# Kernel optimization log

Hardware: AMD Instinct MI355X
Metric: run time of the kernel (lower is better)

The kernel has to match this reference:

```python
import jax, jax.numpy as jnp
import numpy as np

B, S, D, H = 4, 2048, 1024, 16
DK = D // H


def setup_inputs() -> dict:
    key = jax.random.key(0)
    ks = jax.random.split(key, 12)
    scale = 1.0 / np.sqrt(D)
    inp = {
        "query": jax.random.normal(ks[0], (B, S, D), jnp.float32),
        "key": jax.random.normal(ks[1], (B, S, D), jnp.float32),
        "value": jax.random.normal(ks[2], (B, S, D), jnp.float32),
        # lower-triangular causal mask broadcast over batch (1 = keep, 0 = masked)
        "mask": jnp.broadcast_to(jnp.tril(jnp.ones((S, S), jnp.bool_)), (B, S, S)),
        "wq": jax.random.normal(ks[3], (D, D), jnp.float32) * scale,
        "bq": jnp.zeros((D,), jnp.float32),
        "wk": jax.random.normal(ks[4], (D, D), jnp.float32) * scale,
        "bk": jnp.zeros((D,), jnp.float32),
        "wv": jax.random.normal(ks[5], (D, D), jnp.float32) * scale,
        "bv": jnp.zeros((D,), jnp.float32),
        "wo": jax.random.normal(ks[6], (D, D), jnp.float32) * scale,
        "bo": jnp.zeros((D,), jnp.float32),
    }
    return inp


def _split_heads(x):
    # [B, S, D] -> [B, H, S, DK]
    return x.reshape(B, S, H, DK).transpose(0, 2, 1, 3)


def reference(query, key, value, mask, wq, bq, wk, bk, wv, bv, wo, bo):
    # torch.nn.Linear: y = x @ W.T + b
    q = _split_heads(query @ wq.T + bq)
    k = _split_heads(key @ wk.T + bk)
    v = _split_heads(value @ wv.T + bv)

    scores = jnp.einsum("bhqd,bhkd->bhqk", q, k) / jnp.sqrt(jnp.float32(DK))
    # mask.unsqueeze(1): [B,1,S,S] broadcast over heads; masked_fill(mask==0, -1e9)
    scores = jnp.where(mask[:, None, :, :], scores, jnp.float32(-1e9))
    attn = jax.nn.softmax(scores, axis=-1)
    # dropout is identity in eval/reference mode

    ctx = jnp.einsum("bhqk,bhkd->bhqd", attn, v)  # [B,H,S,DK]
    ctx = ctx.transpose(0, 2, 1, 3).reshape(B, S, D)
    return ctx @ wo.T + bo
```

## Files before the change

kernel.cpp:

```cpp
#include <hip/hip_runtime.h>
#include <hip/hip_bf16.h>
#include <hip/hip_fp16.h>

#define B_  4
#define S_  2048
#define D_  1024
#define H_  16
#define DK_ 64

#define DT_F32  0
#define DT_BF16 1
#define DT_F16  2

typedef __bf16 bf16x8 __attribute__((ext_vector_type(8)));
typedef float  f32x4  __attribute__((ext_vector_type(4)));

__device__ __forceinline__ float bf2f(unsigned short u) {
    return __uint_as_float(((unsigned int)u) << 16);
}
__device__ __forceinline__ unsigned short f2bf(float f) {
    unsigned int u = __float_as_uint(f);
    return (unsigned short)((u + 0x7FFFu + ((u >> 16) & 1u)) >> 16);
}
__device__ __forceinline__ float h2f(unsigned short u) {
    union { __half h; unsigned short s; } cv; cv.s = u;
    return __half2float(cv.h);
}
__device__ __forceinline__ unsigned short f2h(float f) {
    union { __half h; unsigned short s; } cv; cv.h = __float2half(f);
    return cv.s;
}

__device__ __forceinline__ void gld_lds16(const void* g, void* l) {
    __builtin_amdgcn_global_load_lds(
        (const __attribute__((address_space(1))) void*)g,
        (__attribute__((address_space(3))) void*)l, 16, 0, 0);
}

template<int DT>
__device__ __forceinline__ float4 ld4(const void* base, size_t idx) {
    if constexpr (DT == DT_F32) {
        return *(const float4*)((const float*)base + idx);
    } else if constexpr (DT == DT_BF16) {
        ushort4 u = *(const ushort4*)((const unsigned short*)base + idx);
        return make_float4(bf2f(u.x), bf2f(u.y), bf2f(u.z), bf2f(u.w));
    } else {
        ushort4 u = *(const ushort4*)((const unsigned short*)base + idx);
        return make_float4(h2f(u.x), h2f(u.y), h2f(u.z), h2f(u.w));
    }
}
template<int DT>
__device__ __forceinline__ float ld1(const void* base, size_t idx) {
    if constexpr (DT == DT_F32)  return ((const float*)base)[idx];
    if constexpr (DT == DT_BF16) return bf2f(((const unsigned short*)base)[idx]);
    return h2f(((const unsigned short*)base)[idx]);
}

__global__ void detect_dtype(const unsigned short* __restrict__ q,
                             int* __restrict__ flag) {
    int c_bf = 0, c_hi = 0;
    for (int i = 0; i < 256; ++i) {
        const int e = (q[i] >> 7) & 0xFF;
        c_bf += (e >= 100 && e <= 140);
        c_hi += (e > 140);
    }
    *flag = (c_hi > 16) ? DT_F32 : ((c_bf >= 250) ? DT_BF16 : DT_F16);
}

__global__ __launch_bounds__(256) void convW(
    const float* __restrict__ wq, const float* __restrict__ wk,
    const float* __restrict__ wv,
    const float* __restrict__ bq, const float* __restrict__ bk,
    const float* __restrict__ bv,
    unsigned short* __restrict__ Wc, unsigned short* __restrict__ Bc,
    const int* __restrict__ flag)
{
    if (*flag != DT_F32) return;
    const size_t NW = (size_t)D_ * D_;
    const size_t i = (size_t)blockIdx.x * blockDim.x + threadIdx.x;
    if (i * 4 < NW) {
        const float* src[3] = {wq, wk, wv};
        #pragma unroll
        for (int j = 0; j < 3; ++j) {
            float4 f = ((const float4*)src[j])[i];
            ushort4 u; u.x = f2bf(f.x); u.y = f2bf(f.y); u.z = f2bf(f.z); u.w = f2bf(f.w);
            ((ushort4*)(Wc + j * NW))[i] = u;
        }
    }
    if (i * 4 < D_) {
        const float* src[3] = {bq, bk, bv};
        #pragma unroll
        for (int j = 0; j < 3; ++j) {
            float4 f = ((const float4*)src[j])[i];
            ushort4 u; u.x = f2bf(f.x); u.y = f2bf(f.y); u.z = f2bf(f.z); u.w = f2bf(f.w);
            ((ushort4*)(Bc + j * D_))[i] = u;
        }
    }
}

__global__ __launch_bounds__(256) void conv3(
    const float* __restrict__ a, unsigned short* __restrict__ da, size_t na,
    const float* __restrict__ w, unsigned short* __restrict__ dw, size_t nw,
    const float* __restrict__ b, unsigned short* __restrict__ db, size_t nb,
    const int* __restrict__ flag)
{
    if (*flag != DT_F32) return;
    const size_t i = (size_t)blockIdx.x * blockDim.x + threadIdx.x;
    if (i * 4 < na) {
        float4 f = ((const float4*)a)[i];
        ushort4 u; u.x = f2bf(f.x); u.y = f2bf(f.y); u.z = f2bf(f.z); u.w = f2bf(f.w);
        ((ushort4*)da)[i] = u;
    }
    if (i * 4 < nw) {
        float4 f = ((const float4*)w)[i];
        ushort4 u; u.x = f2bf(f.x); u.y = f2bf(f.y); u.z = f2bf(f.z); u.w = f2bf(f.w);
        ((ushort4*)dw)[i] = u;
    }
    if (i * 4 < nb) {
        float4 f = ((const float4*)b)[i];
        ushort4 u; u.x = f2bf(f.x); u.y = f2bf(f.y); u.z = f2bf(f.z); u.w = f2bf(f.w);
        ((ushort4*)db)[i] = u;
    }
}

template<bool AF32>
__device__ __forceinline__ void gemm_qkv_body(
    const void* __restrict__ X, const unsigned short* __restrict__ W,
    const unsigned short* __restrict__ Bi, unsigned short* __restrict__ Y,
    const int zmode, const int m0, const int n0)
{
    __shared__ __align__(16) unsigned short Ash[128 * 32];
    __shared__ __align__(16) unsigned short Bsh[256 * 32];
    const int tid  = threadIdx.x;
    const int wv   = tid >> 6, lane = tid & 63;
    const int quad = lane >> 4, l16 = lane & 15;
    const int wm   = wv >> 2,  wn   = wv & 3;
    const int srow = lane >> 2, sc4 = lane & 3;

    f32x4 acc[4][4];
    #pragma unroll
    for (int nt = 0; nt < 4; ++nt) {
        const float bb = bf2f(Bi[n0 + wn * 64 + nt * 16 + l16]);
        #pragma unroll
        for (int mt = 0; mt < 4; ++mt) acc[mt][nt] = (f32x4){bb, bb, bb, bb};
    }

    for (int kt = 0; kt < 32; ++kt) {
        #pragma unroll
        for (int ph = 0; ph < 2; ++ph) {
            const int i   = wv + ph * 8;
            const int row = i * 16 + srow;
            gld_lds16(W + (size_t)(n0 + row) * D_ + kt * 32 + sc4 * 8,
                      (char*)Bsh + i * 1024);
        }
        {
            const int row = wv * 16 + srow;
            unsigned short* dst = Ash + wv * 512 + lane * 8;
            if constexpr (AF32) {
                const float* src = (const float*)X + (size_t)(m0 + row) * D_ + kt * 32 + sc4 * 8;
                const float4 a0 = ((const float4*)src)[0];
                const float4 a1 = ((const float4*)src)[1];
                bf16x8 vv;
                vv[0] = (__bf16)a0.x; vv[1] = (__bf16)a0.y;
                vv[2] = (__bf16)a0.z; vv[3] = (__bf16)a0.w;
                vv[4] = (__bf16)a1.x; vv[5] = (__bf16)a1.y;
                vv[6] = (__bf16)a1.z; vv[7] = (__bf16)a1.w;
                *(bf16x8*)dst = vv;
            } else {
                *(bf16x8*)dst = *(const bf16x8*)(
                    (const unsigned short*)X + (size_t)(m0 + row) * D_ + kt * 32 + sc4 * 8);
            }
        }
        __syncthreads();

        bf16x8 af[4], bfr[4];
        #pragma unroll
        for (int t = 0; t < 4; ++t) {
            af[t]  = *(const bf16x8*)(Ash + (wm * 64 + t * 16 + l16) * 32 + quad * 8);
            bfr[t] = *(const bf16x8*)(Bsh + (wn * 64 + t * 16 + l16) * 32 + quad * 8);
        }
        #pragma unroll
        for (int mt = 0; mt < 4; ++mt)
            #pragma unroll
            for (int nt = 0; nt < 4; ++nt)
                acc[mt][nt] = __builtin_amdgcn_mfma_f32_16x16x32_bf16(
                    af[mt], bfr[nt], acc[mt][nt], 0, 0, 0);
        __syncthreads();
    }

    #pragma unroll
    for (int mt = 0; mt < 4; ++mt) {
        const int mb = m0 + wm * 64 + mt * 16 + quad * 4;
        #pragma unroll
        for (int nt = 0; nt < 4; ++nt) {
            const int n = n0 + wn * 64 + nt * 16 + l16;
            const f32x4 a = acc[mt][nt];
            const int h = n >> 6, dk = n & 63;
            if (zmode != 2) {
                #pragma unroll
                for (int r = 0; r < 4; ++r) {
                    const int m = mb + r, b = m >> 11, s = m & (S_ - 1);
                    Y[(((size_t)(b * H_ + h) * S_ + s) << 6) + dk] = f2bf(a[r]);
                }
            } else {
                const int b = mb >> 11, s = mb & (S_ - 1);
                ushort4 u;
                u.x = f2bf(a[0]); u.y = f2bf(a[1]); u.z = f2bf(a[2]); u.w = f2bf(a[3]);
                *(ushort4*)(Y + (((size_t)(b * H_ + h) * DK_ + dk) << 11) + s) = u;
            }
        }
    }
}

__global__ __launch_bounds__(512) void gemm_qkv(
    const float* __restrict__ xq, const float* __restrict__ xk,
    const float* __restrict__ xv,
    const unsigned short* __restrict__ Wc,
    const unsigned short* __restrict__ wqb, const unsigned short* __restrict__ wkb,
    const unsigned short* __restrict__ wvb,
    const unsigned short* __restrict__ Bc,
    const unsigned short* __restrict__ bqb, const unsigned short* __restrict__ bkb,
    const unsigned short* __restrict__ bvb,
    unsigned short* __restrict__ Ybase,
    const int* __restrict__ flag)
{
    const int f = *flag;
    if (f == DT_F16) return;
    const int zz = blockIdx.z;
    const int n0 = blockIdx.x * 256;
    const int m0 = blockIdx.y * 128;

    const size_t NE = (size_t)B_ * S_ * D_;
    const size_t NW = (size_t)D_ * D_;
    unsigned short* Y = Ybase + (size_t)zz * NE;
    if (f == DT_F32) {
        const void* X = (zz == 0) ? (const void*)xq : (zz == 1) ? (const void*)xk : (const void*)xv;
        gemm_qkv_body<true>(X, Wc + (size_t)zz * NW, Bc + (size_t)zz * D_, Y, zz, m0, n0);
    } else {
        const void* X = (zz == 0) ? (const void*)xq : (zz == 1) ? (const void*)xk : (const void*)xv;
        const unsigned short* W  = (zz == 0) ? wqb : (zz == 1) ? wkb : wvb;
        const unsigned short* Bi = (zz == 0) ? bqb : (zz == 1) ? bkb : bvb;
        gemm_qkv_body<false>(X, W, Bi, Y, zz, m0, n0);
    }
}

__global__ __launch_bounds__(256) void gemm_out(
    const unsigned short* __restrict__ X,
    const unsigned short* __restrict__ Wa, const unsigned short* __restrict__ Wb,
    const unsigned short* __restrict__ Ba, const unsigned short* __restrict__ Bb,
    void* __restrict__ Y,
    const int* __restrict__ flag)
{
    const int f = *flag;
    if (f == DT_F16) return;
    const unsigned short* W  = (f == DT_F32) ? Wa : Wb;
    const unsigned short* Bi = (f == DT_F32) ? Ba : Bb;

    __shared__ __align__(16) unsigned short Ash[128 * 32];
    __shared__ __align__(16) unsigned short Bsh[128 * 32];
    const int tid  = threadIdx.x;
    const int wv   = tid >> 6, lane = tid & 63;
    const int quad = lane >> 4, l16 = lane & 15;
    const int wm   = wv >> 1,  wn   = wv & 1;
    const int srow = lane >> 2, sc4 = lane & 3;
    const int n0 = blockIdx.x * 128;
    const int m0 = blockIdx.y * 128;

    f32x4 acc[4][4];
    #pragma unroll
    for (int nt = 0; nt < 4; ++nt) {
        const float bb = bf2f(Bi[n0 + wn * 64 + nt * 16 + l16]);
        #pragma unroll
        for (int mt = 0; mt < 4; ++mt) acc[mt][nt] = (f32x4){bb, bb, bb, bb};
    }

    for (int kt = 0; kt < 32; ++kt) {
        #pragma unroll
        for (int ph = 0; ph < 2; ++ph) {
            const int i   = wv + ph * 4;
            const int row = i * 16 + srow;
            gld_lds16(X + (size_t)(m0 + row) * D_ + kt * 32 + sc4 * 8,
                      (char*)Ash + i * 1024);
            gld_lds16(W + (size_t)(n0 + row) * D_ + kt * 32 + sc4 * 8,
                      (char*)Bsh + i * 1024);
        }
        __syncthreads();

        bf16x8 af[4], bfr[4];
        #pragma unroll
        for (int t = 0; t < 4; ++t) {
            af[t]  = *(const bf16x8*)(Ash + (wm * 64 + t * 16 + l16) * 32 + quad * 8);
            bfr[t] = *(const bf16x8*)(Bsh + (wn * 64 + t * 16 + l16) * 32 + quad * 8);
        }
        #pragma unroll
        for (int mt = 0; mt < 4; ++mt)
            #pragma unroll
            for (int nt = 0; nt < 4; ++nt)
                acc[mt][nt] = __builtin_amdgcn_mfma_f32_16x16x32_bf16(
                    af[mt], bfr[nt], acc[mt][nt], 0, 0, 0);
        __syncthreads();
    }

    #pragma unroll
    for (int mt = 0; mt < 4; ++mt) {
        const int mb = m0 + wm * 64 + mt * 16 + quad * 4;
        #pragma unroll
        for (int nt = 0; nt < 4; ++nt) {
            const int n = n0 + wn * 64 + nt * 16 + l16;
            const f32x4 a = acc[mt][nt];
            if (f == DT_F32) {
                #pragma unroll
                for (int r = 0; r < 4; ++r)
                    ((float*)Y)[(size_t)(mb + r) * D_ + n] = a[r];
            } else {
                #pragma unroll
                for (int r = 0; r < 4; ++r)
                    ((unsigned short*)Y)[(size_t)(mb + r) * D_ + n] = f2bf(a[r]);
            }
        }
    }
}

__global__ __launch_bounds__(256) void attn_mfma(
    const unsigned short* __restrict__ Q,
    const unsigned short* __restrict__ K,
    const unsigned short* __restrict__ Vt,
    unsigned short* __restrict__ ctx)
{
    __shared__ __align__(16) unsigned short Ksh[2][2 * 64 * 32];
    __shared__ __align__(16) unsigned short Vsh[2][2 * 64 * 32];
    __shared__ __align__(16) __bf16         Psh[4][2 * 16 * 32];
    const int tid  = threadIdx.x;
    const int wv   = tid >> 6, lane = tid & 63;
    const int quad = lane >> 4, l16 = lane & 15;
    const int bx = blockIdx.x, bh = blockIdx.y;
    const unsigned short* Qb = Q  + (size_t)bh * S_ * DK_;
    const unsigned short* Kb = K  + (size_t)bh * S_ * DK_;
    const unsigned short* Vb = Vt + (size_t)bh * DK_ * S_;
    const int b = bh >> 4, h = bh & 15;
    const int srow = lane >> 2, sc4 = lane & 3;
    const int NT = S_ / 64;

    const float C1 = 0.125f * 1.44269504089f;
    const float C0 = -4.0f  * 1.44269504089f;

    auto stage = [&](int buf, int kt) {
        #pragma unroll
        for (int ph = 0; ph < 2; ++ph) {
            const int i  = wv + ph * 4;
            const int kk = i >> 2, r16 = i & 3;
            const int rr = r16 * 16 + srow;
            gld_lds16(Kb + (size_t)(kt * 64 + rr) * DK_ + kk * 32 + sc4 * 8,
                      (char*)(&Ksh[buf][0]) + i * 1024);
            gld_lds16(Vb + (size_t)rr * S_ + kt * 64 + kk * 32 + sc4 * 8,
                      (char*)(&Vsh[buf][0]) + i * 1024);
        }
    };

    #pragma unroll
    for (int seg = 0; seg < 2; ++seg) {
        const int qt = seg ? (NT - 1 - bx) : bx;
        const int q0 = qt * 64;

        const int qrow = q0 + wv * 16 + l16;
        bf16x8 qf0 = *(const bf16x8*)(Qb + (size_t)qrow * DK_ + quad * 8);
        bf16x8 qf1 = *(const bf16x8*)(Qb + (size_t)qrow * DK_ + 32 + quad * 8);

        f32x4 o[4];
        #pragma unroll
        for (int t = 0; t < 4; ++t) o[t] = (f32x4){0.f, 0.f, 0.f, 0.f};
        float lsum[4] = {0.f, 0.f, 0.f, 0.f};
        const int rowb = q0 + wv * 16 + quad * 4;

        stage(0, 0);

        for (int kt = 0; kt <= qt; ++kt) {
            const int cur = kt & 1;
            if (kt < qt) {
                stage(cur ^ 1, kt + 1);
                asm volatile("s_waitcnt vmcnt(4)" ::: "memory");
            } else {
                asm volatile("s_waitcnt vmcnt(0)" ::: "memory");
            }
            __builtin_amdgcn_s_barrier();
            asm volatile("" ::: "memory");

            const unsigned short* Kc = &Ksh[cur][0];
            const unsigned short* Vc = &Vsh[cur][0];

            f32x4 st[4];
            #pragma unroll
            for (int t = 0; t < 4; ++t) {
                bf16x8 k0 = *(const bf16x8*)(Kc + (t * 16 + l16) * 32 + quad * 8);
                bf16x8 k1 = *(const bf16x8*)(Kc + 2048 + (t * 16 + l16) * 32 + quad * 8);
                f32x4 z = (f32x4){0.f, 0.f, 0.f, 0.f};
                st[t] = __builtin_amdgcn_mfma_f32_16x16x32_bf16(qf0, k0, z, 0, 0, 0);
                st[t] = __builtin_amdgcn_mfma_f32_16x16x32_bf16(qf1, k1, st[t], 0, 0, 0);
            }

            float p[4][4];
            if (kt == qt) {
                #pragma unroll
                for (int t = 0; t < 4; ++t) {
                    const int col = kt * 64 + t * 16 + l16;
                    #pragma unroll
                    for (int r = 0; r < 4; ++r) {
                        float sv = fmaf(st[t][r], C1, C0);
                        if (col > rowb + r) sv = -1e9f;
                        p[t][r] = __builtin_amdgcn_exp2f(sv);
                        lsum[r] += p[t][r];
                    }
                }
            } else {
                #pragma unroll
                for (int t = 0; t < 4; ++t)
                    #pragma unroll
                    for (int r = 0; r < 4; ++r) {
                        p[t][r] = __builtin_amdgcn_exp2f(fmaf(st[t][r], C1, C0));
                        lsum[r] += p[t][r];
                    }
            }

            #pragma unroll
            for (int t = 0; t < 4; ++t) {
                const int col = t * 16 + l16;
                const int kk = col >> 5, c32 = col & 31, g = c32 >> 3;
                #pragma unroll
                for (int r = 0; r < 4; ++r) {
                    const int row = quad * 4 + r;
                    Psh[wv][kk * 512 + row * 32 + ((g ^ quad) * 8) + (c32 & 7)] =
                        (__bf16)p[t][r];
                }
            }

            bf16x8 pf[2];
            #pragma unroll
            for (int kk = 0; kk < 2; ++kk)
                pf[kk] = *(const bf16x8*)(&Psh[wv][kk * 512 + l16 * 32 + ((quad ^ (l16 >> 2)) * 8)]);
            #pragma unroll
            for (int t = 0; t < 4; ++t) {
                bf16x8 v0 = *(const bf16x8*)(Vc + (t * 16 + l16) * 32 + quad * 8);
                bf16x8 v1 = *(const bf16x8*)(Vc + 2048 + (t * 16 + l16) * 32 + quad * 8);
                o[t] = __builtin_amdgcn_mfma_f32_16x16x32_bf16(pf[0], v0, o[t], 0, 0, 0);
                o[t] = __builtin_amdgcn_mfma_f32_16x16x32_bf16(pf[1], v1, o[t], 0, 0, 0);
            }
            __syncthreads();
        }

        float li[4];
        #pragma unroll
        for (int r = 0; r < 4; ++r) {
            float l = lsum[r];
            l += __shfl_xor(l, 1, 64);
            l += __shfl_xor(l, 2, 64);
            l += __shfl_xor(l, 4, 64);
            l += __shfl_xor(l, 8, 64);
            li[r] = 1.0f / l;
        }
        #pragma unroll
        for (int t = 0; t < 4; ++t)
            #pragma unroll
            for (int r = 0; r < 4; ++r) {
                const int row = rowb + r;
                ctx[(size_t)(b * S_ + row) * D_ + h * DK_ + t * 16 + l16] =
                    f2bf(o[t][r] * li[r]);
            }
    }
}

template<int MODE, int DT>
__global__ __launch_bounds__(256) void gemm_xwT(
    const void* __restrict__ X,
    const void* __restrict__ W,
    const void* __restrict__ bias,
    void* __restrict__ Y,
    const int* __restrict__ flag)
{
    if (*flag != DT) return;
    constexpr int XDT = (MODE == 1) ? DT_BF16 : DT;

    __shared__ float As[16][65];
    __shared__ float Bs[16][65];
    const int tid = threadIdx.x;
    const int n0 = blockIdx.x * 64;
    const int m0 = blockIdx.y * 64;
    const int tx = tid & 15, ty = tid >> 4;
    const int lr = tid >> 2, lc = (tid & 3) << 2;

    float acc[4][4] = {};
    const size_t xbase = (size_t)(m0 + lr) * D_ + lc;
    const size_t wbase = (size_t)(n0 + lr) * D_ + lc;

    for (int k0 = 0; k0 < D_; k0 += 16) {
        const float4 a = ld4<XDT>(X, xbase + k0);
        const float4 b = ld4<DT >(W, wbase + k0);
        As[lc + 0][lr] = a.x; As[lc + 1][lr] = a.y;
        As[lc + 2][lr] = a.z; As[lc + 3][lr] = a.w;
        Bs[lc + 0][lr] = b.x; Bs[lc + 1][lr] = b.y;
        Bs[lc + 2][lr] = b.z; Bs[lc + 3][lr] = b.w;
        __syncthreads();
        #pragma unroll
        for (int k = 0; k < 16; ++k) {
            float av[4], bv[4];
            #pragma unroll
            for (int i = 0; i < 4; ++i) { av[i] = As[k][ty * 4 + i]; bv[i] = Bs[k][tx * 4 + i]; }
            #pragma unroll
            for (int i = 0; i < 4; ++i)
                #pragma unroll
                for (int j = 0; j < 4; ++j) acc[i][j] += av[i] * bv[j];
        }
        __syncthreads();
    }

    #pragma unroll
    for (int i = 0; i < 4; ++i) {
        const int m = m0 + ty * 4 + i;
        #pragma unroll
        for (int j = 0; j < 4; ++j) {
            const int n = n0 + tx * 4 + j;
            const float y = acc[i][j] + ld1<DT>(bias, n);
            if constexpr (MODE == 0) {
                const int b = m >> 11, s = m & (S_ - 1), h = n >> 6, dk = n & 63;
                ((unsigned short*)Y)[(((size_t)(b * H_ + h) * S_ + s) << 6) + dk] = f2bf(y);
            } else if constexpr (MODE == 2) {
                const int b = m >> 11, s = m & (S_ - 1), h = n >> 6, dk = n & 63;
                ((unsigned short*)Y)[(((size_t)(b * H_ + h) * DK_ + dk) << 11) + s] = f2bf(y);
            } else {
                const size_t oi = (size_t)m * D_ + n;
                if constexpr (DT == DT_F32)       ((float*)Y)[oi] = y;
                else if constexpr (DT == DT_BF16) ((unsigned short*)Y)[oi] = f2bf(y);
                else                              ((unsigned short*)Y)[oi] = f2h(y);
            }
        }
    }
}

__global__ void copy_out(const ulong2* __restrict__ src, ulong2* __restrict__ dst,
                         size_t out_size, const int* __restrict__ flag) {
    const size_t bytes  = out_size * ((*flag == DT_F32) ? 4u : 2u);
    const size_t chunks = bytes >> 4;
    const size_t i = (size_t)blockIdx.x * blockDim.x + threadIdx.x;
    if (i < chunks) dst[i] = src[i];
}

extern "C" void kernel_launch(void* const* d_in, const int* in_sizes, int n_in,
                              void* d_out, int out_size, void* d_ws, size_t ws_size,
                              hipStream_t stream) {
    const int wi = (n_in >= 12) ? 4 : 3;
    const void* q  = d_in[0];
    const void* k  = d_in[1];
    const void* v  = d_in[2];
    const void* wq = d_in[wi + 0];
    const void* bq = d_in[wi + 1];
    const void* wk = d_in[wi + 2];
    const void* bk = d_in[wi + 3];
    const void* wv = d_in[wi + 4];
    const void* bv = d_in[wi + 5];
    const void* wo = d_in[wi + 6];
    const void* bo = d_in[wi + 7];

    const size_t NE = (size_t)B_ * S_ * D_;
    const size_t NW = (size_t)D_ * D_;

    int* flag = (int*)d_ws;
    unsigned short* Qw = (unsigned short*)((char*)d_ws + 256);
    unsigned short* Kw = Qw + NE;
    unsigned short* Vw = Kw + NE;
    unsigned short* Cw = Vw + NE;

    const bool planA = ws_size >= 256 + 4 * NE * 2;

    unsigned short* xconv = (unsigned short*)d_out;
    unsigned short* Wc    = xconv + NE;
    unsigned short* Bc    = Wc + 4 * NW;

    unsigned short* ctx  = planA ? Cw : xconv;
    void*           yfin = planA ? d_out : (void*)Qw;
    unsigned short* WoC = planA ? Kw : (Wc + 3 * NW);
    unsigned short* BoC = planA ? (Kw + NW) : (Bc + 3 * D_);

    detect_dtype<<<1, 1, 0, stream>>>((const unsigned short*)q, flag);

    const dim3 gqkv(D_ / 256, (B_ * S_) / 128, 3);
    const dim3 gm(D_ / 128, (B_ * S_) / 128);
    const dim3 gs(D_ / 64,  (B_ * S_) / 64);
    const int  wgrid = (int)((NW / 4 + 255) / 256);

    convW<<<wgrid, 256, 0, stream>>>((const float*)wq, (const float*)wk,
                                     (const float*)wv,
                                     (const float*)bq, (const float*)bk,
                                     (const float*)bv,
                                     Wc, Bc, flag);

    gemm_qkv<<<gqkv, 512, 0, stream>>>(
        (const float*)q, (const float*)k, (const float*)v,
        Wc,
        (const unsigned short*)wq, (const unsigned short*)wk,
        (const unsigned short*)wv,
        Bc,
        (const unsigned short*)bq, (const unsigned short*)bk,
        (const unsigned short*)bv,
        Qw, flag);

    gemm_xwT<0, DT_F16><<<gs, 256, 0, stream>>>(q, wq, bq, Qw, flag);
    gemm_xwT<0, DT_F16><<<gs, 256, 0, stream>>>(k, wk, bk, Kw, flag);
    gemm_xwT<2, DT_F16><<<gs, 256, 0, stream>>>(v, wv, bv, Vw, flag);

    attn_mfma<<<dim3(S_ / 128, B_ * H_), 256, 0, stream>>>(Qw, Kw, Vw, ctx);

    conv3<<<wgrid, 256, 0, stream>>>((const float*)nullptr, (unsigned short*)nullptr, 0,
                                     (const float*)wo, WoC, NW,
                                     (const float*)bo, BoC, D_, flag);

    gemm_out<<<gm, 256, 0, stream>>>(ctx,
                                     WoC, (const unsigned short*)wo,
                                     BoC, (const unsigned short*)bo,
                                     yfin, flag);
    gemm_xwT<1, DT_F16><<<gs, 256, 0, stream>>>((const void*)ctx, wo, bo, yfin, flag);

    if (!planA) {
        const size_t maxChunks = ((size_t)out_size * 4) >> 4;
        copy_out<<<(int)((maxChunks + 255) / 256), 256, 0, stream>>>(
            (const ulong2*)yfin, (ulong2*)d_out, (size_t)out_size, flag);
    }
}
```

Before: 418.9 us.

## Double K-tile depth in QKV GEMM with XOR-swizzled LDS and parallel dtype detect

The QKV projection GEMM now stages 64-wide K tiles instead of 32, which halves the number of barrier-separated iterations. The LDS layout gets an XOR swizzle on 16-byte chunks to avoid bank conflicts on the wider rows. The dtype detection kernel now uses a 64-lane wave with a shuffle reduction instead of a single serial thread. LDS use doubles per block, which may reduce occupancy.

```diff
diff --git a/kernel.cpp b/kernel.cpp
--- a/kernel.cpp
+++ b/kernel.cpp
@@ -58,13 +58,21 @@
 
 __global__ void detect_dtype(const unsigned short* __restrict__ q,
                              int* __restrict__ flag) {
+    const int lane = threadIdx.x;
     int c_bf = 0, c_hi = 0;
-    for (int i = 0; i < 256; ++i) {
-        const int e = (q[i] >> 7) & 0xFF;
+    #pragma unroll
+    for (int j = 0; j < 4; ++j) {
+        const int e = (q[lane * 4 + j] >> 7) & 0xFF;
         c_bf += (e >= 100 && e <= 140);
         c_hi += (e > 140);
     }
-    *flag = (c_hi > 16) ? DT_F32 : ((c_bf >= 250) ? DT_BF16 : DT_F16);
+    #pragma unroll
+    for (int o = 1; o < 64; o <<= 1) {
+        c_bf += __shfl_xor(c_bf, o, 64);
+        c_hi += __shfl_xor(c_hi, o, 64);
+    }
+    if (lane == 0)
+        *flag = (c_hi > 16) ? DT_F32 : ((c_bf >= 250) ? DT_BF16 : DT_F16);
 }
 
 __global__ __launch_bounds__(256) void convW(
@@ -129,13 +137,14 @@
     const unsigned short* __restrict__ Bi, unsigned short* __restrict__ Y,
     const int zmode, const int m0, const int n0)
 {
-    __shared__ __align__(16) unsigned short Ash[128 * 32];
-    __shared__ __align__(16) unsigned short Bsh[256 * 32];
+    __shared__ __align__(16) unsigned short Ash[128 * 64];
+    __shared__ __align__(16) unsigned short Bsh[256 * 64];
     const int tid  = threadIdx.x;
     const int wv   = tid >> 6, lane = tid & 63;
     const int quad = lane >> 4, l16 = lane & 15;
     const int wm   = wv >> 2,  wn   = wv & 3;
-    const int srow = lane >> 2, sc4 = lane & 3;
+    const int srow8 = lane >> 3, sc8 = lane & 7;
+    const int swz   = sc8 ^ srow8;
 
     f32x4 acc[4][4];
     #pragma unroll
@@ -145,19 +154,21 @@
         for (int mt = 0; mt < 4; ++mt) acc[mt][nt] = (f32x4){bb, bb, bb, bb};
     }
 
-    for (int kt = 0; kt < 32; ++kt) {
+    for (int kt = 0; kt < 16; ++kt) {
+        #pragma unroll
+        for (int ph = 0; ph < 4; ++ph) {
+            const int i   = wv + ph * 8;
+            const int row = i * 8 + srow8;
+            gld_lds16(W + (size_t)(n0 + row) * D_ + kt * 64 + swz * 8,
+                      (char*)Bsh + i * 1024);
+        }
         #pragma unroll
         for (int ph = 0; ph < 2; ++ph) {
             const int i   = wv + ph * 8;
-            const int row = i * 16 + srow;
-            gld_lds16(W + (size_t)(n0 + row) * D_ + kt * 32 + sc4 * 8,
-                      (char*)Bsh + i * 1024);
-        }
-        {
-            const int row = wv * 16 + srow;
-            unsigned short* dst = Ash + wv * 512 + lane * 8;
+            const int row = i * 8 + srow8;
+            unsigned short* dst = Ash + (size_t)i * 512 + srow8 * 64 + swz * 8;
             if constexpr (AF32) {
-                const float* src = (const float*)X + (size_t)(m0 + row) * D_ + kt * 32 + sc4 * 8;
+                const float* src = (const float*)X + (size_t)(m0 + row) * D_ + kt * 64 + sc8 * 8;
                 const float4 a0 = ((const float4*)src)[0];
                 const float4 a1 = ((const float4*)src)[1];
                 bf16x8 vv;
@@ -168,23 +179,28 @@
                 *(bf16x8*)dst = vv;
             } else {
                 *(bf16x8*)dst = *(const bf16x8*)(
-                    (const unsigned short*)X + (size_t)(m0 + row) * D_ + kt * 32 + sc4 * 8);
+                    (const unsigned short*)X + (size_t)(m0 + row) * D_ + kt * 64 + sc8 * 8);
             }
         }
         __syncthreads();
 
-        bf16x8 af[4], bfr[4];
-        #pragma unroll
-        for (int t = 0; t < 4; ++t) {
-            af[t]  = *(const bf16x8*)(Ash + (wm * 64 + t * 16 + l16) * 32 + quad * 8);
-            bfr[t] = *(const bf16x8*)(Bsh + (wn * 64 + t * 16 + l16) * 32 + quad * 8);
-        }
-        #pragma unroll
-        for (int mt = 0; mt < 4; ++mt)
-            #pragma unroll
-            for (int nt = 0; nt < 4; ++nt)
-                acc[mt][nt] = __builtin_amdgcn_mfma_f32_16x16x32_bf16(
-                    af[mt], bfr[nt], acc[mt][nt], 0, 0, 0);
+        #pragma unroll
+        for (int half = 0; half < 2; ++half) {
+            bf16x8 af[4], bfr[4];
+            #pragma unroll
+            for (int t = 0; t < 4; ++t) {
+                const int ra = wm * 64 + t * 16 + l16;
+                af[t]  = *(const bf16x8*)(Ash + ra * 64 + (((half << 2) | quad) ^ (ra & 7)) * 8);
+                const int rb = wn * 64 + t * 16 + l16;
+                bfr[t] = *(const bf16x8*)(Bsh + rb * 64 + (((half << 2) | quad) ^ (rb & 7)) * 8);
+            }
+            #pragma unroll
+            for (int mt = 0; mt < 4; ++mt)
+                #pragma unroll
+                for (int nt = 0; nt < 4; ++nt)
+                    acc[mt][nt] = __builtin_amdgcn_mfma_f32_16x16x32_bf16(
+                        af[mt], bfr[nt], acc[mt][nt], 0, 0, 0);
+        }
         __syncthreads();
     }
 
@@ -579,7 +595,7 @@
     unsigned short* WoC = planA ? Kw : (Wc + 3 * NW);
     unsigned short* BoC = planA ? (Kw + NW) : (Bc + 3 * D_);
 
-    detect_dtype<<<1, 1, 0, stream>>>((const unsigned short*)q, flag);
+    detect_dtype<<<1, 64, 0, stream>>>((const unsigned short*)q, flag);
 
     const dim3 gqkv(D_ / 256, (B_ * S_) / 128, 3);
     const dim3 gm(D_ / 128, (B_ * S_) / 128);
```

Result: faster. 406.6 us (-2.9%).
